# Kernel tuning notes

Hardware: AMD Instinct MI355X
Metric: run time of the kernel (lower is better)

## Reference

```python
import jax, jax.numpy as jnp
import numpy as np

TEMPERATURE = 0.5
NEG_INF_FILL = -1000000000.0


def setup_inputs() -> dict:
    key = jax.random.key(0)
    z = jax.random.normal(key, (16384, 128), dtype=jnp.float32)
    # module expects L2-normalized projected features
    z = z / jnp.linalg.norm(z, axis=-1, keepdims=True)
    return {"z": z}


def reference(z) -> jnp.ndarray:
    N2 = z.shape[0]
    N = N2 // 2
    # (2N, 2N) pairwise similarity scaled by temperature
    sim = (z @ z.T) / TEMPERATURE
    # mask self-similarity on the diagonal
    eye = jnp.eye(N2, dtype=bool)
    sim = jnp.where(eye, NEG_INF_FILL, sim)
    # positive pair index: row i < N pairs with i+N; row i >= N pairs with i-N
    pos_idx = jnp.concatenate([jnp.arange(N, N2), jnp.arange(0, N)])
    positives = sim[jnp.arange(N2), pos_idx]
    loss = -positives + jax.scipy.special.logsumexp(sim, axis=1)
    return loss.mean()
```

## Files before the change

### kernel.cpp

```cpp
#include <hip/hip_runtime.h>
#include <hip/hip_bf16.h>

#define N2    16384
#define NHALF 8192
#define KDIM  128
#define WCOLS 32
#define BCOLS 128
#define NHCOL 8192
#define NITER (NHCOL / BCOLS)

using bf16x8 = __attribute__((ext_vector_type(8))) short;
using f32x4  = __attribute__((ext_vector_type(4))) float;

#if __has_builtin(__builtin_amdgcn_exp2f)
#define EXP2F(x) __builtin_amdgcn_exp2f(x)
#else
#define EXP2F(x) exp2f(x)
#endif
#if __has_builtin(__builtin_amdgcn_logf)
#define LOG2F(x) __builtin_amdgcn_logf(x)
#else
#define LOG2F(x) log2f(x)
#endif

#define PRESCALE 1.6986436005760381f

typedef const __attribute__((address_space(1))) void* gas_ptr;
typedef __attribute__((address_space(3))) void* las_ptr;

__device__ __forceinline__ unsigned short f2bf(float f) {
  unsigned u = __float_as_uint(f);
  u += 0x7fffu + ((u >> 16) & 1u);
  return (unsigned short)(u >> 16);
}

__global__ void k_convert(const float* __restrict__ z, unsigned short* __restrict__ zb,
                          float* __restrict__ S, float* __restrict__ out) {
  int i = blockIdx.x * blockDim.x + threadIdx.x;
  if (i < N2) S[i] = 0.f;
  if (i == 0) out[0] = 0.f;
  float4 v = reinterpret_cast<const float4*>(z)[i];
  ushort4 o;
  o.x = f2bf(v.x * PRESCALE); o.y = f2bf(v.y * PRESCALE);
  o.z = f2bf(v.z * PRESCALE); o.w = f2bf(v.w * PRESCALE);
  reinterpret_cast<ushort4*>(zb)[i] = o;
}

__global__ __launch_bounds__(256, 2) void k_main(const unsigned short* __restrict__ zb,
                                                 float* __restrict__ S) {
  __shared__ __align__(16) unsigned short Bs[4][2][WCOLS * KDIM];
  const int t    = threadIdx.x;
  const int w    = t >> 6;
  const int l    = t & 63;
  const int q    = l >> 4;
  const int c15  = l & 15;
  const int rg   = blockIdx.x >> 1;
  const int half = blockIdx.x & 1;
  const int rbase = rg * 64;

  int srcoff[8];
#pragma unroll
  for (int j = 0; j < 8; ++j) {
    int p   = j * 64 + l;
    int row = p >> 4;
    int pg  = p & 15;
    int k8  = pg ^ (row & 15);
    srcoff[j] = (row * 16 + k8) * 16;
  }

  const char* sbase = (const char*)zb + (size_t)(half * NHCOL + w * WCOLS) * KDIM * 2;

#pragma unroll
  for (int j = 0; j < 8; ++j)
    __builtin_amdgcn_global_load_lds((gas_ptr)(sbase + srcoff[j]),
                                     (las_ptr)(&Bs[w][0][j * 512]), 16, 0, 0);

  bf16x8 afr[4][4];
#pragma unroll
  for (int m = 0; m < 4; ++m) {
    const unsigned short* ap = zb + (size_t)(rbase + m * 16 + c15) * KDIM + q * 8;
#pragma unroll
    for (int s = 0; s < 4; ++s)
      afr[m][s] = *reinterpret_cast<const bf16x8*>(ap + s * 32);
  }
#pragma unroll
  for (int m = 0; m < 4; ++m)
#pragma unroll
    for (int s = 0; s < 4; ++s)
      asm volatile("" : "+v"(afr[m][s]));

  float rowsum[4][4];
#pragma unroll
  for (int m = 0; m < 4; ++m)
#pragma unroll
    for (int r = 0; r < 4; ++r) rowsum[m][r] = 0.f;

  const int dOff0 = (half * NHCOL + w * WCOLS) - rbase;

  f32x4 accA[4][2], accB[4][2];

#define STAGE_BODY(T, CB, NB, ACC, PREFETCH, VMCNT_ASM)                        \
  {                                                                            \
    if (PREFETCH) {                                                            \
      const char* _src = sbase + (size_t)((T) + 1) * BCOLS * KDIM * 2;         \
      _Pragma("unroll")                                                        \
      for (int j = 0; j < 8; ++j)                                              \
        __builtin_amdgcn_global_load_lds((gas_ptr)(_src + srcoff[j]),          \
                                         (las_ptr)(&Bs[w][NB][j * 512]), 16, 0, 0); \
    }                                                                          \
    asm volatile(VMCNT_ASM ::: "memory");                                      \
    bf16x8 bfr[4][2];                                                          \
    _Pragma("unroll")                                                          \
    for (int s = 0; s < 4; ++s)                                                \
      _Pragma("unroll")                                                        \
      for (int n = 0; n < 2; ++n) {                                            \
        int idx = (n * 16 + c15) * KDIM + (((s * 4 + q) ^ c15) * 8);           \
        bfr[s][n] = *reinterpret_cast<const bf16x8*>(&Bs[w][CB][idx]);         \
      }                                                                        \
    _Pragma("unroll")                                                          \
    for (int m = 0; m < 4; ++m)                                                \
      _Pragma("unroll")                                                        \
      for (int n = 0; n < 2; ++n)                                              \
        ACC[m][n] = __builtin_amdgcn_mfma_f32_16x16x32_bf16(                   \
            afr[m][0], bfr[0][n], (f32x4){0.f, 0.f, 0.f, 0.f}, 0, 0, 0);       \
    _Pragma("unroll")                                                          \
    for (int s = 1; s < 4; ++s)                                                \
      _Pragma("unroll")                                                        \
      for (int m = 0; m < 4; ++m)                                              \
        _Pragma("unroll")                                                      \
        for (int n = 0; n < 2; ++n)                                            \
          ACC[m][n] = __builtin_amdgcn_mfma_f32_16x16x32_bf16(                 \
              afr[m][s], bfr[s][n], ACC[m][n], 0, 0, 0);                       \
  }

#define STAGE_P(T, CB, NB, ACC) STAGE_BODY(T, CB, NB, ACC, 1, "s_waitcnt vmcnt(8)")
#define STAGE_L(T, CB, ACC)     STAGE_BODY(T, CB, 0,  ACC, 0, "s_waitcnt vmcnt(0)")

#define EPI(ACC, IT)                                                           \
  {                                                                            \
    const int _dOff = dOff0 + (IT) * BCOLS;                                    \
    _Pragma("unroll")                                                          \
    for (int m = 0; m < 4; ++m)                                                \
      _Pragma("unroll")                                                        \
      for (int n = 0; n < 2; ++n) {                                            \
        const bool dfrag = (_dOff == (m - n) * 16);                            \
        _Pragma("unroll")                                                      \
        for (int r = 0; r < 4; ++r) {                                          \
          float e = EXP2F(ACC[m][n][r]);                                       \
          if (dfrag && (c15 == q * 4 + r)) e = 0.f;                            \
          rowsum[m][r] += e;                                                   \
        }                                                                      \
      }                                                                        \
  }

#define SGB_INTERLEAVE                                                         \
  {                                                                            \
    __builtin_amdgcn_sched_group_barrier(0x100, 8, 0);          \
    _Pragma("unroll")                                                          \
    for (int u = 0; u < 32; ++u) {                                             \
      __builtin_amdgcn_sched_group_barrier(0x008, 1, 0);          \
      __builtin_amdgcn_sched_group_barrier(0x002, 3, 0);          \
    }                                                                          \
  }

  STAGE_P(0, 0, 1, accA);
#pragma unroll 1
  for (int p = 0; p < NITER / 2 - 1; ++p) {
    const int it = 2 * p;
    STAGE_P(it + 1, 1, 0, accB);
    EPI(accA, it);
    SGB_INTERLEAVE;
    STAGE_P(it + 2, 0, 1, accA);
    EPI(accB, it + 1);
    SGB_INTERLEAVE;
  }
  STAGE_L(NITER - 1, 1, accB);
  EPI(accA, NITER - 2);
  SGB_INTERLEAVE;
  EPI(accB, NITER - 1);

#undef STAGE_BODY
#undef STAGE_P
#undef STAGE_L
#undef EPI
#undef SGB_INTERLEAVE

#pragma unroll
  for (int m = 0; m < 4; ++m)
#pragma unroll
    for (int r = 0; r < 4; ++r) {
      float v = rowsum[m][r];
      v += __shfl_xor(v, 1);
      v += __shfl_xor(v, 2);
      v += __shfl_xor(v, 4);
      v += __shfl_xor(v, 8);
      if (c15 == 0) atomicAdd(&S[rbase + m * 16 + q * 4 + r], v);
    }
}

__global__ void k_final(const float* __restrict__ z, const float* __restrict__ S,
                        float* __restrict__ out) {
  __shared__ float red[256];
  int t = threadIdx.x;
  int i = blockIdx.x * 256 + t;
  int j = i ^ NHALF;
  const float4* zi = reinterpret_cast<const float4*>(z + (size_t)i * KDIM);
  const float4* zj = reinterpret_cast<const float4*>(z + (size_t)j * KDIM);
  float dot = 0.f;
#pragma unroll
  for (int k = 0; k < KDIM / 4; ++k) {
    float4 a = zi[k], b = zj[k];
    dot += a.x * b.x + a.y * b.y + a.z * b.z + a.w * b.w;
  }
  float loss = LOG2F(S[i]) * 0.69314718055994531f - 2.f * dot;
  red[t] = loss;
  __syncthreads();
  for (int o = 128; o > 0; o >>= 1) {
    if (t < o) red[t] += red[t + o];
    __syncthreads();
  }
  if (t == 0) atomicAdd(out, red[0] * (1.f / N2));
}

extern "C" void kernel_launch(void* const* d_in, const int* in_sizes, int n_in,
                              void* d_out, int out_size, void* d_ws, size_t ws_size,
                              hipStream_t stream) {
  const float* z = (const float*)d_in[0];
  float* out = (float*)d_out;
  unsigned short* zb = (unsigned short*)d_ws;
  float* S = (float*)((char*)d_ws + (size_t)N2 * KDIM * 2);

  k_convert<<<(N2 * KDIM / 4) / 256, 256, 0, stream>>>(z, zb, S, out);
  k_main<<<(N2 / 64) * 2, 256, 0, stream>>>(zb, S);
  k_final<<<N2 / 256, 256, 0, stream>>>(z, S, out);
}
```

Baseline: 144.5 us.

## Drop in-loop diagonal masking and interleave exp epilogue inside MFMA stages

The diagonal mask check is removed from the main loop. Instead, k_final subtracts the self-similarity term exp2(|zb_i|^2), recomputed from the bf16 row, from the row sum. The exp epilogue for the previous tile is now interleaved per k-slice with the MFMAs of the current tile, using a coarser sched_group_barrier pattern, and the prefetch pointer becomes incremental. This removes the per-element compare from the hot loop and gives the scheduler a tighter overlap of exp and MFMA. The cost is possible precision error from subtracting a large diagonal term, which depends on the bf16 self-dot matching the MFMA result.

```diff
diff --git a/kernel.cpp b/kernel.cpp
--- a/kernel.cpp
+++ b/kernel.cpp
@@ -69,11 +69,13 @@
   }
 
   const char* sbase = (const char*)zb + (size_t)(half * NHCOL + w * WCOLS) * KDIM * 2;
+  const size_t TSTRIDE = (size_t)BCOLS * KDIM * 2;
 
 #pragma unroll
   for (int j = 0; j < 8; ++j)
     __builtin_amdgcn_global_load_lds((gas_ptr)(sbase + srcoff[j]),
                                      (las_ptr)(&Bs[w][0][j * 512]), 16, 0, 0);
+  const char* srcNext = sbase + TSTRIDE;
 
   bf16x8 afr[4][4];
 #pragma unroll
@@ -95,20 +97,20 @@
 #pragma unroll
     for (int r = 0; r < 4; ++r) rowsum[m][r] = 0.f;
 
-  const int dOff0 = (half * NHCOL + w * WCOLS) - rbase;
-
   f32x4 accA[4][2], accB[4][2];
 
-#define STAGE_BODY(T, CB, NB, ACC, PREFETCH, VMCNT_ASM)                        \
+#define STAGE(CB, NB, ACC_W, ACC_R, PRE, DOEPI)                                \
   {                                                                            \
-    if (PREFETCH) {                                                            \
-      const char* _src = sbase + (size_t)((T) + 1) * BCOLS * KDIM * 2;         \
+    if (PRE) {                                                                 \
       _Pragma("unroll")                                                        \
       for (int j = 0; j < 8; ++j)                                              \
-        __builtin_amdgcn_global_load_lds((gas_ptr)(_src + srcoff[j]),          \
+        __builtin_amdgcn_global_load_lds((gas_ptr)(srcNext + srcoff[j]),       \
                                          (las_ptr)(&Bs[w][NB][j * 512]), 16, 0, 0); \
+      srcNext += TSTRIDE;                                                      \
+      asm volatile("s_waitcnt vmcnt(8)" ::: "memory");                         \
+    } else {                                                                   \
+      asm volatile("s_waitcnt vmcnt(0)" ::: "memory");                         \
     }                                                                          \
-    asm volatile(VMCNT_ASM ::: "memory");                                      \
     bf16x8 bfr[4][2];                                                          \
     _Pragma("unroll")                                                          \
     for (int s = 0; s < 4; ++s)                                                \
@@ -118,72 +120,54 @@
         bfr[s][n] = *reinterpret_cast<const bf16x8*>(&Bs[w][CB][idx]);         \
       }                                                                        \
     _Pragma("unroll")                                                          \
-    for (int m = 0; m < 4; ++m)                                                \
-      _Pragma("unroll")                                                        \
-      for (int n = 0; n < 2; ++n)                                              \
-        ACC[m][n] = __builtin_amdgcn_mfma_f32_16x16x32_bf16(                   \
-            afr[m][0], bfr[0][n], (f32x4){0.f, 0.f, 0.f, 0.f}, 0, 0, 0);       \
-    _Pragma("unroll")                                                          \
-    for (int s = 1; s < 4; ++s)                                                \
-      _Pragma("unroll")                                                        \
-      for (int m = 0; m < 4; ++m)                                              \
+    for (int s = 0; s < 4; ++s) {                                              \
+      if (DOEPI) {                                                             \
         _Pragma("unroll")                                                      \
         for (int n = 0; n < 2; ++n)                                            \
-          ACC[m][n] = __builtin_amdgcn_mfma_f32_16x16x32_bf16(                 \
-              afr[m][s], bfr[s][n], ACC[m][n], 0, 0, 0);                       \
-  }
-
-#define STAGE_P(T, CB, NB, ACC) STAGE_BODY(T, CB, NB, ACC, 1, "s_waitcnt vmcnt(8)")
-#define STAGE_L(T, CB, ACC)     STAGE_BODY(T, CB, 0,  ACC, 0, "s_waitcnt vmcnt(0)")
-
-#define EPI(ACC, IT)                                                           \
-  {                                                                            \
-    const int _dOff = dOff0 + (IT) * BCOLS;                                    \
-    _Pragma("unroll")                                                          \
-    for (int m = 0; m < 4; ++m)                                                \
-      _Pragma("unroll")                                                        \
-      for (int n = 0; n < 2; ++n) {                                            \
-        const bool dfrag = (_dOff == (m - n) * 16);                            \
+          _Pragma("unroll")                                                    \
+          for (int r = 0; r < 4; ++r)                                          \
+            rowsum[s][r] += EXP2F(ACC_R[s][n][r]);                             \
+      }                                                                        \
+      if (s == 0) {                                                            \
         _Pragma("unroll")                                                      \
-        for (int r = 0; r < 4; ++r) {                                          \
-          float e = EXP2F(ACC[m][n][r]);                                       \
-          if (dfrag && (c15 == q * 4 + r)) e = 0.f;                            \
-          rowsum[m][r] += e;                                                   \
-        }                                                                      \
+        for (int m = 0; m < 4; ++m)                                            \
+          _Pragma("unroll")                                                    \
+          for (int n = 0; n < 2; ++n)                                          \
+            ACC_W[m][n] = __builtin_amdgcn_mfma_f32_16x16x32_bf16(             \
+                afr[m][0], bfr[0][n], (f32x4){0.f, 0.f, 0.f, 0.f}, 0, 0, 0);   \
+      } else {                                                                 \
+        _Pragma("unroll")                                                      \
+        for (int m = 0; m < 4; ++m)                                            \
+          _Pragma("unroll")                                                    \
+          for (int n = 0; n < 2; ++n)                                          \
+            ACC_W[m][n] = __builtin_amdgcn_mfma_f32_16x16x32_bf16(             \
+                afr[m][s], bfr[s][n], ACC_W[m][n], 0, 0, 0);                   \
       }                                                                        \
-  }
-
-#define SGB_INTERLEAVE                                                         \
-  {                                                                            \
+    }                                                                          \
     __builtin_amdgcn_sched_group_barrier(0x100, 8, 0);          \
     _Pragma("unroll")                                                          \
-    for (int u = 0; u < 32; ++u) {                                             \
-      __builtin_amdgcn_sched_group_barrier(0x008, 1, 0);          \
-      __builtin_amdgcn_sched_group_barrier(0x002, 3, 0);          \
+    for (int u = 0; u < 4; ++u) {                                              \
+      if (DOEPI) __builtin_amdgcn_sched_group_barrier(0x002, 16, 0);           \
+      __builtin_amdgcn_sched_group_barrier(0x008, 8, 0);                       \
     }                                                                          \
   }
 
-  STAGE_P(0, 0, 1, accA);
+  STAGE(0, 1, accA, accA, 1, 0);
 #pragma unroll 1
   for (int p = 0; p < NITER / 2 - 1; ++p) {
-    const int it = 2 * p;
-    STAGE_P(it + 1, 1, 0, accB);
-    EPI(accA, it);
-    SGB_INTERLEAVE;
-    STAGE_P(it + 2, 0, 1, accA);
-    EPI(accB, it + 1);
-    SGB_INTERLEAVE;
-  }
-  STAGE_L(NITER - 1, 1, accB);
-  EPI(accA, NITER - 2);
-  SGB_INTERLEAVE;
-  EPI(accB, NITER - 1);
-
-#undef STAGE_BODY
-#undef STAGE_P
-#undef STAGE_L
-#undef EPI
-#undef SGB_INTERLEAVE
+    STAGE(1, 0, accB, accA, 1, 1);
+    STAGE(0, 1, accA, accB, 1, 1);
+  }
+  STAGE(1, 0, accB, accA, 0, 1);
+#undef STAGE
+
+#pragma unroll
+  for (int m = 0; m < 4; ++m)
+#pragma unroll
+    for (int n = 0; n < 2; ++n)
+#pragma unroll
+      for (int r = 0; r < 4; ++r)
+        rowsum[m][r] += EXP2F(accB[m][n][r]);
 
 #pragma unroll
   for (int m = 0; m < 4; ++m)
@@ -198,8 +182,8 @@
     }
 }
 
-__global__ void k_final(const float* __restrict__ z, const float* __restrict__ S,
-                        float* __restrict__ out) {
+__global__ void k_final(const float* __restrict__ z, const unsigned short* __restrict__ zb,
+                        const float* __restrict__ S, float* __restrict__ out) {
   __shared__ float red[256];
   int t = threadIdx.x;
   int i = blockIdx.x * 256 + t;
@@ -212,7 +196,18 @@
     float4 a = zi[k], b = zj[k];
     dot += a.x * b.x + a.y * b.y + a.z * b.z + a.w * b.w;
   }
-  float loss = LOG2F(S[i]) * 0.69314718055994531f - 2.f * dot;
+  const bf16x8* zr = reinterpret_cast<const bf16x8*>(zb + (size_t)i * KDIM);
+  float d = 0.f;
+#pragma unroll
+  for (int k = 0; k < KDIM / 8; ++k) {
+    bf16x8 v = zr[k];
+#pragma unroll
+    for (int e = 0; e < 8; ++e) {
+      float f = __uint_as_float(((unsigned)(unsigned short)v[e]) << 16);
+      d += f * f;
+    }
+  }
+  float loss = LOG2F(S[i] - EXP2F(d)) * 0.69314718055994531f - 2.f * dot;
   red[t] = loss;
   __syncthreads();
   for (int o = 128; o > 0; o >>= 1) {
@@ -232,5 +227,5 @@
 
   k_convert<<<(N2 * KDIM / 4) / 256, 256, 0, stream>>>(z, zb, S, out);
   k_main<<<(N2 / 64) * 2, 256, 0, stream>>>(zb, S);
-  k_final<<<N2 / 256, 256, 0, stream>>>(z, S, out);
-}
+  k_final<<<N2 / 256, 256, 0, stream>>>(z, zb, S, out);
+}
```

New measurement: 141.6 us. About the same (-2.0%).
